# Kernel optimization log

Measured on AMD Instinct MI355X. Metric: run time of the kernel, lower is better.

The kernel has to match this reference:

```python
import jax, jax.numpy as jnp
import numpy as np

N_HEAD, D_MODEL, DQ, DK, DV = 16, 1024, 64, 64, 64
B, LQ, LK = 2, 2048, 2048
EPS = 1e-3


def setup_inputs() -> dict:
    key = jax.random.key(0)
    ks = jax.random.split(key, 8)
    v = jax.random.normal(ks[0], (B, LK, D_MODEL), jnp.float32)
    k = jax.random.normal(ks[1], (B, LK, D_MODEL), jnp.float32)
    q = jax.random.normal(ks[2], (B, LQ, D_MODEL), jnp.float32)
    mask = jax.random.randint(ks[3], (B, LQ, LK), 0, 2).astype(bool)
    # xavier_normal for [n_head, d_model, d*]: fan_in=d_model, fan_out=d* (per torch, last two dims)
    def xav(kk, shape):
        std = np.sqrt(2.0 / (shape[-2] + shape[-1]))
        return jax.random.normal(kk, shape, jnp.float32) * std
    w_q = xav(ks[4], (N_HEAD, D_MODEL, DQ))
    w_k = xav(ks[5], (N_HEAD, D_MODEL, DK))
    w_v = xav(ks[6], (N_HEAD, D_MODEL, DV))
    # output linear: torch default init; use uniform(-1/sqrt(fan_in), ..)
    fan_in = N_HEAD * DV
    bound = 1.0 / np.sqrt(fan_in)
    kw, kb = jax.random.split(ks[7])
    w_o = jax.random.uniform(kw, (fan_in, D_MODEL), jnp.float32, -bound, bound)
    b_o = jax.random.uniform(kb, (D_MODEL,), jnp.float32, -bound, bound)
    gamma = jnp.ones((D_MODEL,), jnp.float32)
    beta = jnp.zeros((D_MODEL,), jnp.float32)
    return {"v": v, "k": k, "q": q, "mask": mask, "w_q": w_q, "w_k": w_k,
            "w_v": w_v, "w_o": w_o, "b_o": b_o, "gamma": gamma, "beta": beta}


def _layer_norm(x, gamma, beta):
    mean = jnp.mean(x, axis=-1, keepdims=True)
    # torch.std default is unbiased (ddof=1); eps added to std (not var)
    std = jnp.std(x, axis=-1, keepdims=True, ddof=1)
    return (x - mean) / (std + EPS) * gamma + beta


def reference(v, k, q, mask, w_q, w_k, w_v, w_o, b_o, gamma, beta):
    residual = k  # source uses k as residual
    # per-head projections: [h, b, l, d*]
    qh = jnp.einsum('bld,hde->hble', q, w_q)
    kh = jnp.einsum('bld,hde->hble', k, w_k)
    vh = jnp.einsum('bld,hde->hble', v, w_v)
    scale = 1.0 / np.sqrt(DK)
    scores = jnp.einsum('hbqe,hbke->hbqk', qh, kh) * scale  # [h,b,Lq,Lk]
    scores = jnp.where(mask[None], -jnp.inf, scores)
    attn = jax.nn.softmax(scores, axis=-1)
    out = jnp.einsum('hbqk,hbke->hbqe', attn, vh)  # [h,b,Lq,dv]
    # cat(split(out, batch, dim=0), dim=-1): heads concatenated on last dim
    out = out.transpose(1, 2, 0, 3).reshape(out.shape[1], out.shape[2], -1)
    out = out @ w_o + b_o
    x = out + residual  # dropout is identity in eval
    return _layer_norm(x, gamma, beta)
```

## Files before the change

kernel.cpp:

```cpp
#include <hip/hip_runtime.h>
#include <math.h>

typedef __bf16 bf16_t;
typedef bf16_t bf16x8 __attribute__((ext_vector_type(8)));
typedef float  f32x4  __attribute__((ext_vector_type(4)));
typedef unsigned short u16;
typedef u16 ushortx4 __attribute__((ext_vector_type(4)));
typedef unsigned long long u64;

#define MFMA16(a, b, c) __builtin_amdgcn_mfma_f32_16x16x32_bf16((a), (b), (c), 0, 0, 0)

__device__ __forceinline__ u16 f2bf(float f) {
    unsigned int u = __float_as_uint(f);
    u = (u + 0x7fffu + ((u >> 16) & 1u)) >> 16;
    return (u16)u;
}

__device__ __forceinline__ float bf2f(unsigned int u) {
    return __uint_as_float(u << 16);
}

__device__ __forceinline__ void gld16(const u16* g, u16* l) {
    __builtin_amdgcn_global_load_lds(
        (const __attribute__((address_space(1))) void*)g,
        (__attribute__((address_space(3))) void*)l, 16, 0, 0);
}


__global__ __launch_bounds__(256) void k_prep(const float* __restrict__ q,
                                              const float* __restrict__ k,
                                              const float* __restrict__ v,
                                              const int* __restrict__ mask,
                                              const float* __restrict__ w_q,
                                              const float* __restrict__ w_k,
                                              const float* __restrict__ w_v,
                                              const float* __restrict__ w_o,
                                              u16* __restrict__ qb,
                                              u16* __restrict__ kb,
                                              u16* __restrict__ vb,
                                              u64* __restrict__ mask64,
                                              u16* __restrict__ wqt,
                                              u16* __restrict__ wkt,
                                              u16* __restrict__ wvt,
                                              u16* __restrict__ wot) {
    __shared__ float tile[32][33];
    int bid = blockIdx.x;
    if (bid < 12288) {
        int sel = bid >> 12;
        int i = (bid & 4095) * 256 + threadIdx.x;
        const float* src = sel == 0 ? q : (sel == 1 ? k : v);
        u16* dst = sel == 0 ? qb : (sel == 1 ? kb : vb);
        float4 val = ((const float4*)src)[i];
        ushortx4 r;
        r[0] = f2bf(val.x); r[1] = f2bf(val.y); r[2] = f2bf(val.z); r[3] = f2bf(val.w);
        ((ushortx4*)dst)[i] = r;
    } else if (bid < 20480) {
        int b2 = bid - 12288;
        int ktg = b2 & 7, q4 = (b2 >> 3) & 511, b = b2 >> 12;
        int wave = threadIdx.x >> 6, lane = threadIdx.x & 63;
        int qq = q4 * 4 + wave;
        const int* mp = mask + ((size_t)(b * 2048 + qq)) * 2048 + ktg * 256 + lane;
#pragma unroll
        for (int i = 0; i < 4; ++i) {
            int m = mp[i * 64];
            u64 bal = __ballot(m != 0);
            if (lane == 0) mask64[((size_t)(b * 32 + ktg * 4 + i)) * 2048 + qq] = bal;
        }
    } else {
        int b3 = bid - 20480;
        const float* src;
        u16* dst;
        int r0, c0, C;
        if (b3 < 3072) {
            int x = b3 & 31, y = (b3 >> 5) & 1, z = b3 >> 6;
            int h = z & 15, sel = z >> 4;
            src = (sel == 0 ? w_q : (sel == 1 ? w_k : w_v)) + (size_t)h * 65536;
            dst = (sel == 0 ? wqt : (sel == 1 ? wkt : wvt)) + (size_t)h * 65536;
            r0 = x * 32; c0 = y * 32; C = 64;
        } else {
            int t = b3 - 3072;
            r0 = (t & 31) * 32; c0 = (t >> 5) * 32; C = 1024;
            src = w_o; dst = wot;
        }
        int tx = threadIdx.x & 31, ty = threadIdx.x >> 5;
        const float* s = src + ((size_t)r0) * C + c0;
#pragma unroll
        for (int i = 0; i < 4; ++i) tile[ty + i * 8][tx] = s[(ty + i * 8) * (size_t)C + tx];
        __syncthreads();
        u16* d = dst + ((size_t)c0) * 1024 + r0;
#pragma unroll
        for (int i = 0; i < 4; ++i) d[(ty + i * 8) * 1024 + tx] = f2bf(tile[tx][ty + i * 8]);
    }
}

#define GEMM_CORE(Ablk, Bblk, ACC)                                                    \
    int c0 = wave * 2;                                                                \
    const u16* Ag0 = Ablk + (size_t)(c0 * 16 + l15) * 1024 + quad * 8;                \
    const u16* Ag1 = Ablk + (size_t)((c0 + 1) * 16 + l15) * 1024 + quad * 8;          \
    const u16* Bg0 = Bblk + (size_t)(c0 * 16 + l15) * 1024 + quad * 8;                \
    const u16* Bg1 = Bblk + (size_t)((c0 + 1) * 16 + l15) * 1024 + quad * 8;          \
    gld16(Ag0, As + c0 * 512); gld16(Ag1, As + (c0 + 1) * 512);                       \
    gld16(Bg0, Bs + c0 * 512); gld16(Bg1, Bs + (c0 + 1) * 512);                       \
    __syncthreads();                                                                  \
    int buf = 0;                                                                      \
    for (int ks = 0; ks < 32; ++ks) {                                                 \
        if (ks < 31) {                                                                \
            int k0 = (ks + 1) * 32;                                                   \
            gld16(Ag0 + k0, As + (buf ^ 1) * 4096 + c0 * 512);                        \
            gld16(Ag1 + k0, As + (buf ^ 1) * 4096 + (c0 + 1) * 512);                  \
            gld16(Bg0 + k0, Bs + (buf ^ 1) * 4096 + c0 * 512);                        \
            gld16(Bg1 + k0, Bs + (buf ^ 1) * 4096 + (c0 + 1) * 512);                  \
        }                                                                             \
        bf16x8 af[4], bfr[4];                                                         \
        _Pragma("unroll")                                                             \
        for (int i = 0; i < 4; ++i)                                                   \
            af[i] = *(const bf16x8*)(As + buf * 4096 + (wy * 4 + i) * 512 + lane * 8);\
        _Pragma("unroll")                                                             \
        for (int j = 0; j < 4; ++j)                                                   \
            bfr[j] = *(const bf16x8*)(Bs + buf * 4096 + (wx * 4 + j) * 512 + lane * 8);\
        _Pragma("unroll")                                                             \
        for (int i = 0; i < 4; ++i)                                                   \
            _Pragma("unroll")                                                         \
            for (int j = 0; j < 4; ++j) ACC[i][j] = MFMA16(af[i], bfr[j], ACC[i][j]); \
        __syncthreads();                                                              \
        buf ^= 1;                                                                     \
    }

__global__ __launch_bounds__(256) void k_proj(
    const u16* __restrict__ qb, const u16* __restrict__ kb, const u16* __restrict__ vb,
    const u16* __restrict__ wqt, const u16* __restrict__ wkt, const u16* __restrict__ wvt,
    u16* __restrict__ oq, u16* __restrict__ okh, u16* __restrict__ ovt) {
    __shared__ __align__(16) u16 smem[18432];
    u16* As = smem;
    u16* Bs = smem + 8192;
    int z = blockIdx.y, gx = blockIdx.x;
    int bm, bn;
    const u16 *A, *B;
    if (z == 0)      { bm = gx & 31; bn = gx >> 5; A = qb; B = wqt; }
    else if (z == 1) { bm = gx & 31; bn = gx >> 5; A = kb; B = wkt; }
    else             { bn = gx & 31; bm = gx >> 5; A = wvt; B = vb; }
    A += (size_t)bm * 128 * 1024;
    B += (size_t)bn * 128 * 1024;
    int tid = threadIdx.x, wave = tid >> 6, lane = tid & 63;
    int wy = wave >> 1, wx = wave & 1, l15 = lane & 15, quad = lane >> 4;
    f32x4 acc[4][4] = {};
    GEMM_CORE(A, B, acc)
    u16* ep = smem + wave * 4608;
    float mulf = (z == 0) ? 0.18033688011112042f : 1.0f;
#pragma unroll
    for (int i = 0; i < 4; ++i)
#pragma unroll
        for (int j = 0; j < 4; ++j)
#pragma unroll
            for (int r = 0; r < 4; ++r)
                ep[(i * 16 + quad * 4 + r) * 72 + j * 16 + l15] = f2bf(acc[i][j][r] * mulf);
    int rl = lane >> 3, cg = lane & 7;
    if (z < 2) {
        int hh = bn * 2 + wx;
        int m0 = bm * 128 + wy * 64;
        int bb = m0 >> 11, l0 = m0 & 2047;
        u16* O = (z ? okh : oq) + ((size_t)((hh * 2 + bb) * 2048 + l0)) * 64;
#pragma unroll
        for (int s = 0; s < 8; ++s) {
            int row = s * 8 + rl;
            uint4 v = *(const uint4*)(ep + row * 72 + cg * 8);
            *(uint4*)(O + (size_t)row * 64 + cg * 8) = v;
        }
    } else {
        int m0 = bm * 128 + wy * 64;
        int hh = m0 >> 6;
        int n0 = bn * 128 + wx * 64;
        int bb = n0 >> 11, l0 = n0 & 2047;
        u16* O = ovt + (size_t)(hh * 2 + bb) * 131072 + (size_t)(m0 & 63) * 2048 + l0;
#pragma unroll
        for (int s = 0; s < 8; ++s) {
            int row = s * 8 + rl;
            uint4 v = *(const uint4*)(ep + row * 72 + cg * 8);
            *(uint4*)(O + (size_t)row * 2048 + cg * 8) = v;
        }
    }
}

__global__ __launch_bounds__(256) void k_attn(
    const u16* __restrict__ qh, const u16* __restrict__ kh,
    const u16* __restrict__ vt, const u64* __restrict__ mask64,
    u16* __restrict__ po, float* __restrict__ pl) {
    int hb = blockIdx.x, qt = blockIdx.y, ksp = blockIdx.z;
    int b = hb & 1;
    int tid = threadIdx.x, wave = tid >> 6, lane = tid & 63;
    int l15 = lane & 15, quad = lane >> 4;

    __shared__ __align__(16) u16 Ks[2][4096], Vs[2][4096];
    __shared__ __align__(16) u16 Pb[4][1024];

    int qrow0 = qt * 128 + wave * 32;
    const u16* Qp = qh + ((size_t)(hb * 2048) + qrow0 + l15) * 64 + quad * 8;
    bf16x8 qf[2][2];
    qf[0][0] = *(const bf16x8*)Qp;
    qf[0][1] = *(const bf16x8*)(Qp + 32);
    qf[1][0] = *(const bf16x8*)(Qp + 1024);
    qf[1][1] = *(const bf16x8*)(Qp + 1024 + 32);

    int c0 = wave * 2;
    const u16* Kg0 = kh + (size_t)hb * 131072 + (size_t)ksp * 65536 +
                     (size_t)(wave * 16 + l15) * 64 + quad * 8;
    const u16* Kg1 = Kg0 + 32;
    const u16* Vg0 = vt + (size_t)hb * 131072 + (size_t)(wave * 16 + l15) * 2048 +
                     ksp * 1024 + quad * 8;
    const u16* Vg1 = Vg0 + 32;
    const u64* Mp = mask64 + (size_t)b * 65536 + (size_t)ksp * 32768 + qrow0 + l15;

    float l_lane[2] = {0.f, 0.f};
    f32x4 o[2][4] = {};

    gld16(Kg0, &Ks[0][c0 * 512]);
    gld16(Kg1, &Ks[0][(c0 + 1) * 512]);
    gld16(Vg0, &Vs[0][c0 * 512]);
    gld16(Vg1, &Vs[0][(c0 + 1) * 512]);
    u64 mw0 = Mp[0], mw1 = Mp[16];
    __syncthreads();
    int buf = 0;
    int swz = (l15 & 7) << 3;
    for (int kt = 0; kt < 16; ++kt) {
        u64 mwn0 = 0, mwn1 = 0;
        if (kt < 15) {
            gld16(Kg0 + (size_t)(kt + 1) * 4096, &Ks[buf ^ 1][c0 * 512]);
            gld16(Kg1 + (size_t)(kt + 1) * 4096, &Ks[buf ^ 1][(c0 + 1) * 512]);
            gld16(Vg0 + (size_t)(kt + 1) * 64, &Vs[buf ^ 1][c0 * 512]);
            gld16(Vg1 + (size_t)(kt + 1) * 64, &Vs[buf ^ 1][(c0 + 1) * 512]);
            mwn0 = Mp[(size_t)(kt + 1) * 2048];
            mwn1 = Mp[(size_t)(kt + 1) * 2048 + 16];
        }
        bf16x8 kf[8], vf[8];
#pragma unroll
        for (int c = 0; c < 8; ++c) kf[c] = *(const bf16x8*)&Ks[buf][c * 512 + lane * 8];
#pragma unroll
        for (int c = 0; c < 8; ++c) vf[c] = *(const bf16x8*)&Vs[buf][c * 512 + lane * 8];
#pragma unroll
        for (int hf = 0; hf < 2; ++hf) {
            u64 mw = hf ? mw1 : mw0;
            f32x4 st[4] = {};
#pragma unroll
            for (int t = 0; t < 4; ++t) {
                st[t] = MFMA16(kf[t * 2], qf[hf][0], st[t]);
                st[t] = MFMA16(kf[t * 2 + 1], qf[hf][1], st[t]);
            }
            unsigned int w0 = (unsigned int)(mw >> (quad * 4));
            unsigned int w1 = (unsigned int)(mw >> (32 + quad * 4));
#pragma unroll
            for (int r = 0; r < 4; ++r) {
                st[0][r] = ((w0 >> r) & 1u) ? -3e30f : st[0][r];
                st[1][r] = ((w0 >> (16 + r)) & 1u) ? -3e30f : st[1][r];
                st[2][r] = ((w1 >> r) & 1u) ? -3e30f : st[2][r];
                st[3][r] = ((w1 >> (16 + r)) & 1u) ? -3e30f : st[3][r];
            }
            float ll = 0.f;
#pragma unroll
            for (int t = 0; t < 4; ++t) {
                float p0 = __builtin_amdgcn_exp2f(st[t][0]);
                float p1 = __builtin_amdgcn_exp2f(st[t][1]);
                float p2 = __builtin_amdgcn_exp2f(st[t][2]);
                float p3 = __builtin_amdgcn_exp2f(st[t][3]);
                ll += (p0 + p1) + (p2 + p3);
                uint2 pk;
                pk.x = (__float_as_uint(p1) & 0xffff0000u) | (__float_as_uint(p0) >> 16);
                pk.y = (__float_as_uint(p3) & 0xffff0000u) | (__float_as_uint(p2) >> 16);
                int g = t * 2 + (quad >> 1);
                int phys = l15 * 64 + (((g << 3) ^ swz)) + (quad & 1) * 4;
                *(uint2*)&Pb[wave][phys] = pk;
            }
            l_lane[hf] += ll;
#pragma unroll
            for (int kc = 0; kc < 2; ++kc) {
                int g = kc * 4 + quad;
                bf16x8 pf = *(const bf16x8*)&Pb[wave][l15 * 64 + (((g << 3) ^ swz))];
#pragma unroll
                for (int t = 0; t < 4; ++t)
                    o[hf][t] = MFMA16(pf, vf[t * 2 + kc], o[hf][t]);
            }
        }
        mw0 = mwn0; mw1 = mwn1;
        __syncthreads();
        buf ^= 1;
    }
    size_t rowbase = ((size_t)ksp * 32 + hb) * 2048 + qrow0;
    int rl = lane >> 3, cg = lane & 7;
#pragma unroll
    for (int hf = 0; hf < 2; ++hf) {
        float ls = l_lane[hf];
        ls += __shfl_xor(ls, 16, 64);
        ls += __shfl_xor(ls, 32, 64);
        if (quad == 0) pl[rowbase + hf * 16 + l15] = ls;
#pragma unroll
        for (int t = 0; t < 4; ++t)
#pragma unroll
            for (int r = 0; r < 4; ++r) {
                int row = quad * 4 + r, col = t * 16 + l15;
                int g = col >> 3;
                Pb[wave][row * 64 + (((g ^ (row & 7)) << 3)) + (col & 7)] =
                    f2bf(o[hf][t][r]);
            }
#pragma unroll
        for (int s = 0; s < 2; ++s) {
            int row = s * 8 + rl;
            uint4 v = *(const uint4*)&Pb[wave][row * 64 + ((cg ^ (row & 7)) << 3)];
            *(uint4*)(po + (rowbase + hf * 16 + row) * 64 + cg * 8) = v;
        }
    }
}

__global__ __launch_bounds__(256) void k_amerge(const u16* __restrict__ po,
                                                const float* __restrict__ pl,
                                                u16* __restrict__ ao) {
    int bid = blockIdx.x;
    int hb = bid >> 6, rc = bid & 63;
    int h = hb >> 1, b = hb & 1;
    int tid = threadIdx.x;
    int r = tid >> 3, c = tid & 7;
    int row = rc * 32 + r;
    size_t i0 = ((size_t)hb * 2048 + row) * 64 + c * 8;
    uint4 a0 = *(const uint4*)(po + i0);
    uint4 a1 = *(const uint4*)(po + i0 + 4194304);
    float l0 = pl[(size_t)hb * 2048 + row];
    float l1 = pl[65536 + (size_t)hb * 2048 + row];
    float inv = 1.0f / (l0 + l1);
    unsigned int* pa0 = (unsigned int*)&a0;
    unsigned int* pa1 = (unsigned int*)&a1;
    uint4 out;
    unsigned int* po_ = (unsigned int*)&out;
#pragma unroll
    for (int i = 0; i < 4; ++i) {
        float lo = (bf2f(pa0[i] & 0xffffu) + bf2f(pa1[i] & 0xffffu)) * inv;
        float hi = (bf2f(pa0[i] >> 16) + bf2f(pa1[i] >> 16)) * inv;
        po_[i] = (unsigned int)f2bf(lo) | ((unsigned int)f2bf(hi) << 16);
    }
    *(uint4*)(ao + ((size_t)(b * 2048 + row)) * 1024 + h * 64 + c * 8) = out;
}

__global__ __launch_bounds__(512) void k_out(
    const u16* __restrict__ ao, const u16* __restrict__ wot,
    float* __restrict__ xp0, float* __restrict__ xp1) {
    __shared__ __align__(16) u16 smem[18432];
    u16* As = smem;
    u16* Bs = smem + 8192;
    int gx = blockIdx.x, bm = gx & 31, bn = gx >> 5;
    int ksp = blockIdx.y;
    const u16* A = ao + (size_t)bm * 128 * 1024 + ksp * 512;
    const u16* B = wot + (size_t)bn * 128 * 1024 + ksp * 512;
    float* xp = ksp ? xp1 : xp0;
    int tid = threadIdx.x, wave = tid >> 6, lane = tid & 63;
    int wy = wave >> 2, wx = wave & 3, l15 = lane & 15, quad = lane >> 4;
    const u16* Ag = A + (size_t)(wave * 16 + l15) * 1024 + quad * 8;
    const u16* Bg = B + (size_t)(wave * 16 + l15) * 1024 + quad * 8;
    f32x4 acc[4][2] = {};
    gld16(Ag, As + wave * 512);
    gld16(Bg, Bs + wave * 512);
    __syncthreads();
    int buf = 0;
    for (int ks = 0; ks < 16; ++ks) {
        if (ks < 15) {
            int k0 = (ks + 1) * 32;
            gld16(Ag + k0, As + (buf ^ 1) * 4096 + wave * 512);
            gld16(Bg + k0, Bs + (buf ^ 1) * 4096 + wave * 512);
        }
        bf16x8 af[4], bfr[2];
#pragma unroll
        for (int i = 0; i < 4; ++i)
            af[i] = *(const bf16x8*)(As + buf * 4096 + (wy * 4 + i) * 512 + lane * 8);
#pragma unroll
        for (int j = 0; j < 2; ++j)
            bfr[j] = *(const bf16x8*)(Bs + buf * 4096 + (wx * 2 + j) * 512 + lane * 8);
#pragma unroll
        for (int i = 0; i < 4; ++i)
#pragma unroll
            for (int j = 0; j < 2; ++j) acc[i][j] = MFMA16(af[i], bfr[j], acc[i][j]);
        __syncthreads();
        buf ^= 1;
    }
    float* epf = (float*)smem + wave * 1152;
    int rl = lane >> 3, cg = lane & 7;
    int mbase = bm * 128 + wy * 64, nbase = bn * 128 + wx * 32;
#pragma unroll
    for (int cc = 0; cc < 2; ++cc) {
#pragma unroll
        for (int i2 = 0; i2 < 2; ++i2)
#pragma unroll
            for (int j = 0; j < 2; ++j)
#pragma unroll
                for (int r = 0; r < 4; ++r)
                    epf[(i2 * 16 + quad * 4 + r) * 36 + j * 16 + l15] =
                        acc[cc * 2 + i2][j][r];
#pragma unroll
        for (int s = 0; s < 4; ++s) {
            int row = s * 8 + rl;
            f32x4 v = *(const f32x4*)(epf + row * 36 + cg * 4);
            int m = mbase + cc * 32 + row, n = nbase + cg * 4;
            *(f32x4*)(xp + (size_t)m * 1024 + n) = v;
        }
    }
}

__global__ __launch_bounds__(256) void k_ln(const float* __restrict__ xp0,
                                            const float* __restrict__ xp1,
                                            const float* __restrict__ resid,
                                            const float* __restrict__ bo,
                                            const float* __restrict__ gamma,
                                            const float* __restrict__ beta,
                                            float* __restrict__ out) {
    int row = blockIdx.x;
    size_t base = (size_t)row * 256;
    float4 a0 = ((const float4*)xp0)[base + threadIdx.x];
    float4 a1 = ((const float4*)xp1)[base + threadIdx.x];
    float4 rs = ((const float4*)resid)[base + threadIdx.x];
    float4 b4 = ((const float4*)bo)[threadIdx.x];
    float4 v;
    v.x = a0.x + a1.x + rs.x + b4.x;
    v.y = a0.y + a1.y + rs.y + b4.y;
    v.z = a0.z + a1.z + rs.z + b4.z;
    v.w = a0.w + a1.w + rs.w + b4.w;
    float s = v.x + v.y + v.z + v.w;
    float ss = v.x * v.x + v.y * v.y + v.z * v.z + v.w * v.w;
#pragma unroll
    for (int off = 32; off; off >>= 1) {
        s += __shfl_down(s, off, 64);
        ss += __shfl_down(ss, off, 64);
    }
    __shared__ float sb[8];
    int wave = threadIdx.x >> 6, lane = threadIdx.x & 63;
    if (lane == 0) { sb[wave] = s; sb[4 + wave] = ss; }
    __syncthreads();
    s = sb[0] + sb[1] + sb[2] + sb[3];
    ss = sb[4] + sb[5] + sb[6] + sb[7];
    float mean = s * (1.0f / 1024.0f);
    float var = fmaxf((ss - 1024.0f * mean * mean) * (1.0f / 1023.0f), 0.f);
    float inv = 1.0f / (sqrtf(var) + 1e-3f);
    float4 g = ((const float4*)gamma)[threadIdx.x];
    float4 bt = ((const float4*)beta)[threadIdx.x];
    float4 o;
    o.x = (v.x - mean) * inv * g.x + bt.x;
    o.y = (v.y - mean) * inv * g.y + bt.y;
    o.z = (v.z - mean) * inv * g.z + bt.z;
    o.w = (v.w - mean) * inv * g.w + bt.w;
    ((float4*)(out))[base + threadIdx.x] = o;
}

extern "C" void kernel_launch(void* const* d_in, const int* in_sizes, int n_in,
                              void* d_out, int out_size, void* d_ws, size_t ws_size,
                              hipStream_t stream) {
    const float* v_in  = (const float*)d_in[0];
    const float* k_in  = (const float*)d_in[1];
    const float* q_in  = (const float*)d_in[2];
    const int*   mask  = (const int*)d_in[3];
    const float* w_q   = (const float*)d_in[4];
    const float* w_k   = (const float*)d_in[5];
    const float* w_v   = (const float*)d_in[6];
    const float* w_o   = (const float*)d_in[7];
    const float* b_o   = (const float*)d_in[8];
    const float* gamma = (const float*)d_in[9];
    const float* beta  = (const float*)d_in[10];
    float* out = (float*)d_out;

    char* ws = (char*)d_ws;
    const size_t MB = 1ull << 20;
    u16* qb  = (u16*)(ws + 0 * MB);
    u16* kb  = (u16*)(ws + 8 * MB);
    u16* vb  = (u16*)(ws + 16 * MB);
    u16* wqt = (u16*)(ws + 24 * MB);
    u16* wkt = (u16*)(ws + 26 * MB);
    u16* wvt = (u16*)(ws + 28 * MB);
    u16* wot = (u16*)(ws + 30 * MB);
    u16* qh  = (u16*)(ws + 32 * MB);
    u16* kh  = (u16*)(ws + 40 * MB);
    u16* vt  = (u16*)(ws + 48 * MB);
    u16* ao  = (u16*)(ws + 56 * MB);
    u64* mask64 = (u64*)(ws + 64 * MB);
    u16*   po = (u16*)(ws + 0 * MB);
    float* pl = (float*)(ws + 16 * MB);
    float* xp0 = (float*)(ws + 32 * MB);
    float* xp1 = (float*)(ws + 64 * MB);

    k_prep<<<dim3(24576), dim3(256), 0, stream>>>(q_in, k_in, v_in, mask,
                                                  w_q, w_k, w_v, w_o,
                                                  qb, kb, vb, mask64,
                                                  wqt, wkt, wvt, wot);
    k_proj<<<dim3(256, 3), dim3(256), 0, stream>>>(qb, kb, vb, wqt, wkt, wvt, qh, kh, vt);
    k_attn<<<dim3(32, 16, 2), dim3(256), 0, stream>>>(qh, kh, vt, mask64, po, pl);
    k_amerge<<<dim3(2048), dim3(256), 0, stream>>>(po, pl, ao);
    k_out<<<dim3(256, 2), dim3(512), 0, stream>>>(ao, wot, xp0, xp1);
    k_ln<<<dim3(4096), dim3(256), 0, stream>>>(xp0, xp1, k_in, b_o, gamma, beta, out);
}
```

Measured before the change: 300.6 us.

## Permute K row loading so P stays in registers for the PV MFMA

```diff
diff --git a/kernel.cpp b/kernel.cpp
--- a/kernel.cpp
+++ b/kernel.cpp
@@ -191,7 +191,7 @@
     int l15 = lane & 15, quad = lane >> 4;
 
     __shared__ __align__(16) u16 Ks[2][4096], Vs[2][4096];
-    __shared__ __align__(16) u16 Pb[4][1024];
+    __shared__ __align__(16) u16 Eb[4][1024];
 
     int qrow0 = qt * 128 + wave * 32;
     const u16* Qp = qh + ((size_t)(hb * 2048) + qrow0 + l15) * 64 + quad * 8;
@@ -202,8 +202,9 @@
     qf[1][1] = *(const bf16x8*)(Qp + 1024 + 32);
 
     int c0 = wave * 2;
+    int rowp = (wave >> 1) * 32 + (l15 >> 2) * 8 + (wave & 1) * 4 + (l15 & 3);
     const u16* Kg0 = kh + (size_t)hb * 131072 + (size_t)ksp * 65536 +
-                     (size_t)(wave * 16 + l15) * 64 + quad * 8;
+                     (size_t)rowp * 64 + quad * 8;
     const u16* Kg1 = Kg0 + 32;
     const u16* Vg0 = vt + (size_t)hb * 131072 + (size_t)(wave * 16 + l15) * 2048 +
                      ksp * 1024 + quad * 8;
@@ -220,7 +221,6 @@
     u64 mw0 = Mp[0], mw1 = Mp[16];
     __syncthreads();
     int buf = 0;
-    int swz = (l15 & 7) << 3;
     for (int kt = 0; kt < 16; ++kt) {
         u64 mwn0 = 0, mwn1 = 0;
         if (kt < 15) {
@@ -245,16 +245,17 @@
                 st[t] = MFMA16(kf[t * 2], qf[hf][0], st[t]);
                 st[t] = MFMA16(kf[t * 2 + 1], qf[hf][1], st[t]);
             }
-            unsigned int w0 = (unsigned int)(mw >> (quad * 4));
-            unsigned int w1 = (unsigned int)(mw >> (32 + quad * 4));
+            unsigned int w0 = (unsigned int)(mw >> (quad * 8));
+            unsigned int w1 = (unsigned int)(mw >> (32 + quad * 8));
 #pragma unroll
             for (int r = 0; r < 4; ++r) {
                 st[0][r] = ((w0 >> r) & 1u) ? -3e30f : st[0][r];
-                st[1][r] = ((w0 >> (16 + r)) & 1u) ? -3e30f : st[1][r];
+                st[1][r] = ((w0 >> (4 + r)) & 1u) ? -3e30f : st[1][r];
                 st[2][r] = ((w1 >> r) & 1u) ? -3e30f : st[2][r];
-                st[3][r] = ((w1 >> (16 + r)) & 1u) ? -3e30f : st[3][r];
+                st[3][r] = ((w1 >> (4 + r)) & 1u) ? -3e30f : st[3][r];
             }
             float ll = 0.f;
+            unsigned int pw[8];
 #pragma unroll
             for (int t = 0; t < 4; ++t) {
                 float p0 = __builtin_amdgcn_exp2f(st[t][0]);
@@ -262,21 +263,17 @@
                 float p2 = __builtin_amdgcn_exp2f(st[t][2]);
                 float p3 = __builtin_amdgcn_exp2f(st[t][3]);
                 ll += (p0 + p1) + (p2 + p3);
-                uint2 pk;
-                pk.x = (__float_as_uint(p1) & 0xffff0000u) | (__float_as_uint(p0) >> 16);
-                pk.y = (__float_as_uint(p3) & 0xffff0000u) | (__float_as_uint(p2) >> 16);
-                int g = t * 2 + (quad >> 1);
-                int phys = l15 * 64 + (((g << 3) ^ swz)) + (quad & 1) * 4;
-                *(uint2*)&Pb[wave][phys] = pk;
+                pw[t * 2]     = (__float_as_uint(p1) & 0xffff0000u) | (__float_as_uint(p0) >> 16);
+                pw[t * 2 + 1] = (__float_as_uint(p3) & 0xffff0000u) | (__float_as_uint(p2) >> 16);
             }
             l_lane[hf] += ll;
-#pragma unroll
-            for (int kc = 0; kc < 2; ++kc) {
-                int g = kc * 4 + quad;
-                bf16x8 pf = *(const bf16x8*)&Pb[wave][l15 * 64 + (((g << 3) ^ swz))];
-#pragma unroll
-                for (int t = 0; t < 4; ++t)
-                    o[hf][t] = MFMA16(pf, vf[t * 2 + kc], o[hf][t]);
+            union { unsigned int w[4]; bf16x8 v; } p0u, p1u;
+            p0u.w[0] = pw[0]; p0u.w[1] = pw[1]; p0u.w[2] = pw[2]; p0u.w[3] = pw[3];
+            p1u.w[0] = pw[4]; p1u.w[1] = pw[5]; p1u.w[2] = pw[6]; p1u.w[3] = pw[7];
+#pragma unroll
+            for (int t = 0; t < 4; ++t) {
+                o[hf][t] = MFMA16(p0u.v, vf[t * 2], o[hf][t]);
+                o[hf][t] = MFMA16(p1u.v, vf[t * 2 + 1], o[hf][t]);
             }
         }
         mw0 = mwn0; mw1 = mwn1;
@@ -297,13 +294,13 @@
             for (int r = 0; r < 4; ++r) {
                 int row = quad * 4 + r, col = t * 16 + l15;
                 int g = col >> 3;
-                Pb[wave][row * 64 + (((g ^ (row & 7)) << 3)) + (col & 7)] =
+                Eb[wave][row * 64 + ((g ^ (row & 7)) << 3) + (col & 7)] =
                     f2bf(o[hf][t][r]);
             }
 #pragma unroll
         for (int s = 0; s < 2; ++s) {
             int row = s * 8 + rl;
-            uint4 v = *(const uint4*)&Pb[wave][row * 64 + ((cg ^ (row & 7)) << 3)];
+            uint4 v = *(const uint4*)&Eb[wave][row * 64 + ((cg ^ (row & 7)) << 3)];
             *(uint4*)(po + (rowbase + hf * 16 + row) * 64 + cg * 8) = v;
         }
     }
```

Result: faster. 293.2 us (-2.5%).
